# Kernel optimization log

Measured on AMD Instinct MI355X. Metric: run time of the kernel, lower is better.

The kernel has to match this reference:

```python
import jax, jax.numpy as jnp
import numpy as np

NEG_SLOPE = 0.2

def gat_layer(x, W, al, ar, src, dst, n_dst):
    # x: [Ns, Fin]; W: [Fin, H*D]; al/ar: [H, D]; src/dst: [E]
    H, D = al.shape
    h = (x @ W).reshape(-1, H, D)          # [Ns, H, D]
    h_dst = h[:n_dst]                       # dst nodes are prefix of src nodes (DGL block)
    el = (h * al).sum(-1)                   # [Ns, H]
    er = (h_dst * ar).sum(-1)               # [Nd, H]
    e = jax.nn.leaky_relu(el[src] + er[dst], NEG_SLOPE)  # [E, H]
    m = jax.ops.segment_max(e, dst, num_segments=n_dst)  # stable edge-softmax
    a = jnp.exp(e - m[dst])
    s = jax.ops.segment_sum(a, dst, num_segments=n_dst)
    alpha = a / s[dst]                      # [E, H]
    msg = h[src] * alpha[:, :, None]        # [E, H, D]
    out = jax.ops.segment_sum(msg, dst, num_segments=n_dst)  # [Nd, H, D]
    return out.reshape(n_dst, H * D)


def setup_inputs() -> dict:
    key = jax.random.key(0)
    ks = jax.random.split(key, 16)
    N0, N1, N2, N3 = 200000, 100000, 50000, 25000
    E0, E1, E2 = 1000000, 500000, 250000
    Fin, Dh, H, C = 256, 64, 3, 40
    inp = {}
    inp['x'] = jax.random.normal(ks[0], (N0, Fin), jnp.float32)
    inp['src0'] = jax.random.randint(ks[1], (E0,), 0, N0, jnp.int32)
    inp['dst0'] = jnp.sort(jax.random.randint(ks[2], (E0,), 0, N1, jnp.int32))
    inp['src1'] = jax.random.randint(ks[3], (E1,), 0, N1, jnp.int32)
    inp['dst1'] = jnp.sort(jax.random.randint(ks[4], (E1,), 0, N2, jnp.int32))
    inp['src2'] = jax.random.randint(ks[5], (E2,), 0, N2, jnp.int32)
    inp['dst2'] = jnp.sort(jax.random.randint(ks[6], (E2,), 0, N3, jnp.int32))
    sc = lambda f: np.float32(1.0 / np.sqrt(f))
    inp['W0'] = jax.random.normal(ks[7], (Fin, H * Dh), jnp.float32) * sc(Fin)
    inp['al0'] = jax.random.normal(ks[8], (H, Dh), jnp.float32) * sc(Dh)
    inp['ar0'] = jax.random.normal(ks[9], (H, Dh), jnp.float32) * sc(Dh)
    inp['W1'] = jax.random.normal(ks[10], (H * Dh, H * Dh), jnp.float32) * sc(H * Dh)
    inp['al1'] = jax.random.normal(ks[11], (H, Dh), jnp.float32) * sc(Dh)
    inp['ar1'] = jax.random.normal(ks[12], (H, Dh), jnp.float32) * sc(Dh)
    inp['W2'] = jax.random.normal(ks[13], (H * Dh, C), jnp.float32) * sc(H * Dh)
    inp['al2'] = jax.random.normal(ks[14], (1, C), jnp.float32) * sc(C)
    inp['ar2'] = jax.random.normal(ks[15], (1, C), jnp.float32) * sc(C)
    return inp


def reference(x, src0, dst0, src1, dst1, src2, dst2,
              W0, al0, ar0, W1, al1, ar1, W2, al2, ar2):
    N1, N2, N3 = 100000, 50000, 25000
    h = gat_layer(x, W0, al0, ar0, src0, dst0, N1)
    h = jax.nn.relu(h)  # dropout is identity in eval/deterministic mode
    h = gat_layer(h, W1, al1, ar1, src1, dst1, N2)
    h = jax.nn.relu(h)
    out = gat_layer(h, W2, al2, ar2, src2, dst2, N3)  # [N3, n_classes]
    return out
```

## Files before the change

### kernel.cpp

```cpp
#include <hip/hip_runtime.h>
#include <math.h>

#define DEV_INLINE __device__ __forceinline__

typedef __attribute__((ext_vector_type(8))) short short8v;
typedef __attribute__((ext_vector_type(4))) float float4v;

DEV_INLINE unsigned short f2bf_rtn(float f) {
  unsigned u = __float_as_uint(f);
  u += 0x7FFFu + ((u >> 16) & 1u);
  return (unsigned short)(u >> 16);
}
DEV_INLINE float bf2f(unsigned short s) { return __uint_as_float(((unsigned)s) << 16); }

DEV_INLINE int soff(int row, int oct) { return row * 32 + ((oct ^ ((row >> 1) & 3)) << 3); }

__global__ void conv_w_all(const float* __restrict__ W0, const float* __restrict__ W1,
                           const float* __restrict__ W2, short* __restrict__ w0h,
                           short* __restrict__ w0l, short* __restrict__ w1h,
                           short* __restrict__ w1l, short* __restrict__ w2h,
                           short* __restrict__ w2l) {
  const int S0 = 256 * 192, S1 = 192 * 192, S2 = 192 * 40;
  int idx = blockIdx.x * 256 + threadIdx.x;
  const float* W; short *Wh, *Wl; int K;
  if (idx < S0) { W = W0; Wh = w0h; Wl = w0l; K = 256; }
  else if (idx < S0 + S1) { idx -= S0; W = W1; Wh = w1h; Wl = w1l; K = 192; }
  else if (idx < S0 + S1 + S2) { idx -= S0 + S1; W = W2; Wh = w2h; Wl = w2l; K = 192; }
  else return;
  int n = idx / K, k = idx - n * K;
  int N = (W == W0 || W == W1) ? 192 : 40;
  float w = W[(size_t)k * N + n];
  unsigned short h = f2bf_rtn(w);
  Wh[idx] = (short)h;
  Wl[idx] = (short)f2bf_rtn(w - bf2f(h));
}

__global__ void csr_all(const int* __restrict__ d0, const int* __restrict__ d1,
                        const int* __restrict__ d2, int* __restrict__ o0,
                        int* __restrict__ o1, int* __restrict__ o2,
                        int E0, int E1, int E2, int n1, int n2, int n3) {
  int i = blockIdx.x * 256 + threadIdx.x;
  const int* dst; int* off; int E, nd;
  if (i < E0) { dst = d0; off = o0; E = E0; nd = n1; }
  else if (i < E0 + E1) { i -= E0; dst = d1; off = o1; E = E1; nd = n2; }
  else if (i < E0 + E1 + E2) { i -= E0 + E1; dst = d2; off = o2; E = E2; nd = n3; }
  else return;
  int d = dst[i];
  int p = (i == 0) ? -1 : dst[i - 1];
  for (int q = p + 1; q <= d; ++q) off[q] = i;
  if (i == E - 1)
    for (int q = d + 1; q <= nd; ++q) off[q] = E;
}

#define ISSUE_B(k0)                                                           \
  {                                                                           \
    _Pragma("unroll")                                                         \
    for (int q = 0; q < BREP; ++q) {                                          \
      int n = sr + q * 64;                                                    \
      if (n < BN) {                                                           \
        if (n < N) {                                                          \
          pbh[q] = *(const short8v*)(Bth + (size_t)n * K + (k0) + oct * 8);   \
          pbl[q] = *(const short8v*)(Btl + (size_t)n * K + (k0) + oct * 8);   \
        } else {                                                              \
          _Pragma("unroll")                                                   \
          for (int j = 0; j < 8; ++j) { pbh[q][j] = 0; pbl[q][j] = 0; }       \
        }                                                                     \
      }                                                                       \
    }                                                                         \
  }

#define STAGE_B(buf)                                                          \
  {                                                                           \
    _Pragma("unroll")                                                         \
    for (int q = 0; q < BREP; ++q) {                                          \
      int n = sr + q * 64;                                                    \
      if (n < BN) {                                                           \
        *(short8v*)(Bs_h[buf] + soff(n, oct)) = pbh[q];                       \
        *(short8v*)(Bs_l[buf] + soff(n, oct)) = pbl[q];                       \
      }                                                                       \
    }                                                                         \
  }

template <int NT, int H>
__global__ __launch_bounds__(256) void gemm_fused(
    const float* __restrict__ A, const short* __restrict__ Bth,
    const short* __restrict__ Btl, const float* __restrict__ al,
    const float* __restrict__ ar, float* __restrict__ C,
    float* __restrict__ el, float* __restrict__ er,
    int M, int N, int K, int n_dst) {
  constexpr int BN = NT * 16;
  constexpr int BREP = (BN + 63) / 64;
  constexpr int TPH = NT / H;
  __shared__ short Bs_h[2][BN * 32], Bs_l[2][BN * 32];
  const int tid = threadIdx.x;
  const int w = tid >> 6, lane = tid & 63;
  const int quad = lane >> 4, l16 = lane & 15;
  const int m0 = blockIdx.x * 128;

  float4v acc[2][NT];
#pragma unroll
  for (int mt = 0; mt < 2; ++mt)
#pragma unroll
    for (int nt = 0; nt < NT; ++nt)
#pragma unroll
      for (int r = 0; r < 4; ++r) acc[mt][nt][r] = 0.f;

  const int sr = tid >> 2;
  const int oct = tid & 3;

  short8v pbh[BREP], pbl[BREP];

  const int nk = K >> 5;
  ISSUE_B(0);
  STAGE_B(0);
  if (nk > 1) ISSUE_B(32);
  __syncthreads();

  for (int kt = 0; kt < nk; ++kt) {
    const int cur = kt & 1;
    const int k0 = kt << 5;
    float4 fA[2][2];
#pragma unroll
    for (int mt = 0; mt < 2; ++mt) {
      int row = m0 + w * 32 + mt * 16 + l16;
      if (row < M) {
        const float* ap = A + (size_t)row * K + k0 + quad * 8;
        fA[mt][0] = *(const float4*)ap;
        fA[mt][1] = *(const float4*)(ap + 4);
      } else {
        fA[mt][0] = make_float4(0.f, 0.f, 0.f, 0.f);
        fA[mt][1] = fA[mt][0];
      }
    }
    if (kt + 1 < nk) STAGE_B(cur ^ 1);
    if (kt + 2 < nk) ISSUE_B((kt + 2) << 5);
    short8v afh[2], afl[2];
#pragma unroll
    for (int mt = 0; mt < 2; ++mt) {
      float vs[8] = {fA[mt][0].x, fA[mt][0].y, fA[mt][0].z, fA[mt][0].w,
                     fA[mt][1].x, fA[mt][1].y, fA[mt][1].z, fA[mt][1].w};
#pragma unroll
      for (int j = 0; j < 8; ++j) {
        unsigned short hh = f2bf_rtn(vs[j]);
        afh[mt][j] = (short)hh;
        afl[mt][j] = (short)f2bf_rtn(vs[j] - bf2f(hh));
      }
    }
#pragma unroll
    for (int nt = 0; nt < NT; ++nt) {
      int col = nt * 16 + l16;
      short8v bfh = *(const short8v*)(Bs_h[cur] + soff(col, quad));
      short8v bfl = *(const short8v*)(Bs_l[cur] + soff(col, quad));
#pragma unroll
      for (int mt = 0; mt < 2; ++mt) {
        acc[mt][nt] = __builtin_amdgcn_mfma_f32_16x16x32_bf16(afh[mt], bfh, acc[mt][nt], 0, 0, 0);
        acc[mt][nt] = __builtin_amdgcn_mfma_f32_16x16x32_bf16(afh[mt], bfl, acc[mt][nt], 0, 0, 0);
        acc[mt][nt] = __builtin_amdgcn_mfma_f32_16x16x32_bf16(afl[mt], bfh, acc[mt][nt], 0, 0, 0);
      }
    }
    if (kt + 1 < nk) __syncthreads();
  }

  float av[NT], rv[NT];
#pragma unroll
  for (int nt = 0; nt < NT; ++nt) {
    int col = nt * 16 + l16;
    av[nt] = (col < N) ? al[col] : 0.f;
    rv[nt] = (col < N) ? ar[col] : 0.f;
  }
#pragma unroll
  for (int mt = 0; mt < 2; ++mt)
#pragma unroll
    for (int r = 0; r < 4; ++r) {
      int gm = m0 + w * 32 + mt * 16 + quad * 4 + r;
      if (gm >= M) continue;
      float pl[H], pr[H];
#pragma unroll
      for (int h = 0; h < H; ++h) { pl[h] = 0.f; pr[h] = 0.f; }
#pragma unroll
      for (int nt = 0; nt < NT; ++nt) {
        int h = nt / TPH;
        pl[h] = fmaf(acc[mt][nt][r], av[nt], pl[h]);
        pr[h] = fmaf(acc[mt][nt][r], rv[nt], pr[h]);
      }
#pragma unroll
      for (int h = 0; h < H; ++h) {
#pragma unroll
        for (int o = 8; o >= 1; o >>= 1) {
          pl[h] += __shfl_xor(pl[h], o, 16);
          pr[h] += __shfl_xor(pr[h], o, 16);
        }
      }
      if (l16 == 0) {
#pragma unroll
        for (int h = 0; h < H; ++h) {
          el[gm * H + h] = pl[h];
          if (gm < n_dst) er[gm * H + h] = pr[h];
        }
      }
#pragma unroll
      for (int nt = 0; nt < NT; ++nt) {
        int col = nt * 16 + l16;
        if (col < N) C[(size_t)gm * N + col] = acc[mt][nt][r];
      }
    }
}

template <int H, int D, bool RELU>
__global__ __launch_bounds__(256) void agg2_kernel(
    const float* __restrict__ hsrc, const float* __restrict__ el,
    const float* __restrict__ er, const int* __restrict__ src,
    const int* __restrict__ off, float* __restrict__ out, int n_dst) {
  constexpr int F = H * D;
  constexpr int NP = (F + 63) / 64;
  __shared__ float wbuf[16][16][H];
  __shared__ int sbuf[16][16];
  const int g = threadIdx.x >> 4, l = threadIdx.x & 15;
  const int d = blockIdx.x * 16 + g;
  if (d >= n_dst) return;
  const int lo = off[d], hi = off[d + 1];

  if (hi <= lo) {
#pragma unroll
    for (int p = 0; p < NP; ++p) {
      int c4 = (p * 16 + l) * 4;
      if (c4 < F) *(float4*)(out + (size_t)d * F + c4) = make_float4(0.f, 0.f, 0.f, 0.f);
    }
    return;
  }

  float erv[H], s_part[H];
#pragma unroll
  for (int h = 0; h < H; ++h) {
    erv[h] = er[d * H + h];
    s_part[h] = 0.f;
  }
  float4 acc[NP];
#pragma unroll
  for (int p = 0; p < NP; ++p) acc[p] = make_float4(0.f, 0.f, 0.f, 0.f);

  for (int base = lo; base < hi; base += 16) {
    const int i = base + l;
    const bool valid = i < hi;
    const int sid = valid ? src[i] : 0;
#pragma unroll
    for (int h = 0; h < H; ++h) {
      float e = 0.f;
      if (valid) {
        e = el[sid * H + h] + erv[h];
        e = e > 0.f ? e : 0.2f * e;
        e = __expf(e);
      }
      s_part[h] += e;
      wbuf[g][l][h] = e;
    }
    sbuf[g][l] = sid;

    const int cnt = min(16, hi - base);
    int sj = sbuf[g][0];
    float4 hv[NP], hn[NP];
#pragma unroll
    for (int p = 0; p < NP; ++p) {
      int c4 = (p * 16 + l) * 4;
      hv[p] = (c4 < F) ? *(const float4*)(hsrc + (size_t)sj * F + c4)
                       : make_float4(0.f, 0.f, 0.f, 0.f);
    }
    for (int ei = 0; ei < cnt; ++ei) {
      if (ei + 1 < cnt) {
        int sj2 = sbuf[g][ei + 1];
#pragma unroll
        for (int p = 0; p < NP; ++p) {
          int c4 = (p * 16 + l) * 4;
          hn[p] = (c4 < F) ? *(const float4*)(hsrc + (size_t)sj2 * F + c4)
                           : make_float4(0.f, 0.f, 0.f, 0.f);
        }
      }
#pragma unroll
      for (int p = 0; p < NP; ++p) {
        int c4 = (p * 16 + l) * 4;
        float wc = wbuf[g][ei][c4 / D];
        acc[p].x = fmaf(wc, hv[p].x, acc[p].x);
        acc[p].y = fmaf(wc, hv[p].y, acc[p].y);
        acc[p].z = fmaf(wc, hv[p].z, acc[p].z);
        acc[p].w = fmaf(wc, hv[p].w, acc[p].w);
      }
#pragma unroll
      for (int p = 0; p < NP; ++p) hv[p] = hn[p];
    }
  }

#pragma unroll
  for (int h = 0; h < H; ++h)
#pragma unroll
    for (int o = 8; o >= 1; o >>= 1) s_part[h] += __shfl_xor(s_part[h], o, 16);

#pragma unroll
  for (int p = 0; p < NP; ++p) {
    int c4 = (p * 16 + l) * 4;
    if (c4 < F) {
      float inv = 1.f / s_part[c4 / D];
      float4 o;
      o.x = acc[p].x * inv; o.y = acc[p].y * inv;
      o.z = acc[p].z * inv; o.w = acc[p].w * inv;
      if (RELU) {
        o.x = fmaxf(o.x, 0.f); o.y = fmaxf(o.y, 0.f);
        o.z = fmaxf(o.z, 0.f); o.w = fmaxf(o.w, 0.f);
      }
      *(float4*)(out + (size_t)d * F + c4) = o;
    }
  }
}

extern "C" void kernel_launch(void* const* d_in, const int* in_sizes, int n_in,
                              void* d_out, int out_size, void* d_ws, size_t ws_size,
                              hipStream_t stream) {
  const float* x   = (const float*)d_in[0];
  const int* src0  = (const int*)d_in[1];
  const int* dst0  = (const int*)d_in[2];
  const int* src1  = (const int*)d_in[3];
  const int* dst1  = (const int*)d_in[4];
  const int* src2  = (const int*)d_in[5];
  const int* dst2  = (const int*)d_in[6];
  const float* W0  = (const float*)d_in[7];
  const float* al0 = (const float*)d_in[8];
  const float* ar0 = (const float*)d_in[9];
  const float* W1  = (const float*)d_in[10];
  const float* al1 = (const float*)d_in[11];
  const float* ar1 = (const float*)d_in[12];
  const float* W2  = (const float*)d_in[13];
  const float* al2 = (const float*)d_in[14];
  const float* ar2 = (const float*)d_in[15];

  const int N0 = 200000, N1 = 100000, N2 = 50000, N3 = 25000;
  const int E0 = in_sizes[1], E1 = in_sizes[3], E2 = in_sizes[5];
  const int Fin = 256, F = 192, C = 40;

  float* ws     = (float*)d_ws;
  float* h_buf  = ws;
  float* o_buf  = h_buf + (size_t)N0 * F;
  float* el_buf = o_buf + (size_t)N1 * F;
  float* er_buf = el_buf + (size_t)N0 * 3;
  short* w0h    = (short*)(er_buf + (size_t)N1 * 3);
  short* w0l    = w0h + 192 * 256;
  short* w1h    = w0l + 192 * 256;
  short* w1l    = w1h + 192 * 192;
  short* w2h    = w1l + 192 * 192;
  short* w2l    = w2h + 40 * 192;
  int*   off0   = (int*)(w2l + 40 * 192);
  int*   off1   = off0 + (N1 + 1);
  int*   off2   = off1 + (N2 + 1);

  dim3 blk(256);

  const int WTOT = 256 * 192 + 192 * 192 + 192 * 40;
  conv_w_all<<<dim3((WTOT + 255) / 256), blk, 0, stream>>>(W0, W1, W2, w0h, w0l, w1h, w1l, w2h, w2l);
  const int ETOT = E0 + E1 + E2;
  csr_all<<<dim3((ETOT + 255) / 256), blk, 0, stream>>>(dst0, dst1, dst2, off0, off1, off2,
                                                        E0, E1, E2, N1, N2, N3);

  gemm_fused<12, 3><<<dim3((N0 + 127) / 128), blk, 0, stream>>>(
      x, w0h, w0l, al0, ar0, h_buf, el_buf, er_buf, N0, F, Fin, N1);
  agg2_kernel<3, 64, true><<<dim3((N1 + 15) / 16), blk, 0, stream>>>(
      h_buf, el_buf, er_buf, src0, off0, o_buf, N1);

  gemm_fused<12, 3><<<dim3((N1 + 127) / 128), blk, 0, stream>>>(
      o_buf, w1h, w1l, al1, ar1, h_buf, el_buf, er_buf, N1, F, F, N2);
  agg2_kernel<3, 64, true><<<dim3((N2 + 15) / 16), blk, 0, stream>>>(
      h_buf, el_buf, er_buf, src1, off1, o_buf, N2);

  gemm_fused<3, 1><<<dim3((N2 + 127) / 128), blk, 0, stream>>>(
      o_buf, w2h, w2l, al2, ar2, h_buf, el_buf, er_buf, N2, C, F, N3);
  agg2_kernel<1, 40, false><<<dim3((N3 + 15) / 16), blk, 0, stream>>>(
      h_buf, el_buf, er_buf, src2, off2, (float*)d_out, N3);
}
```

Baseline: 662.4 us.

## Load GEMM weight tiles directly into LDS via global_load_lds DMA

Replaces the register-staged B-tile loads (global to registers, then registers to LDS, with two-deep prefetch) with direct global-to-LDS loads using global_load_lds. The swizzle is folded into the per-lane global offset. The last-layer weights are padded to 48 columns so the DMA needs no bounds check. It also adds an occupancy hint of 3 blocks per CU, aiming to cut register pressure and LDS store instructions. The prefetch depth drops to one tile, and correctness depends on the hidden sync and swizzle matching the LDS layout.

```diff
diff --git a/kernel.cpp b/kernel.cpp
--- a/kernel.cpp
+++ b/kernel.cpp
@@ -14,21 +14,29 @@
 DEV_INLINE float bf2f(unsigned short s) { return __uint_as_float(((unsigned)s) << 16); }
 
 DEV_INLINE int soff(int row, int oct) { return row * 32 + ((oct ^ ((row >> 1) & 3)) << 3); }
+
+DEV_INLINE void gload_lds16(const void* g, void* l) {
+  __builtin_amdgcn_global_load_lds(
+      (const __attribute__((address_space(1))) void*)g,
+      (__attribute__((address_space(3))) void*)l, 16, 0, 0);
+}
 
 __global__ void conv_w_all(const float* __restrict__ W0, const float* __restrict__ W1,
                            const float* __restrict__ W2, short* __restrict__ w0h,
                            short* __restrict__ w0l, short* __restrict__ w1h,
                            short* __restrict__ w1l, short* __restrict__ w2h,
                            short* __restrict__ w2l) {
-  const int S0 = 256 * 192, S1 = 192 * 192, S2 = 192 * 40;
+  const int S0 = 256 * 192, S1 = 192 * 192, S2 = 192 * 48;
   int idx = blockIdx.x * 256 + threadIdx.x;
   const float* W; short *Wh, *Wl; int K;
-  if (idx < S0) { W = W0; Wh = w0h; Wl = w0l; K = 256; }
-  else if (idx < S0 + S1) { idx -= S0; W = W1; Wh = w1h; Wl = w1l; K = 192; }
-  else if (idx < S0 + S1 + S2) { idx -= S0 + S1; W = W2; Wh = w2h; Wl = w2l; K = 192; }
+  int which;
+  if (idx < S0) { W = W0; Wh = w0h; Wl = w0l; K = 256; which = 0; }
+  else if (idx < S0 + S1) { idx -= S0; W = W1; Wh = w1h; Wl = w1l; K = 192; which = 1; }
+  else if (idx < S0 + S1 + S2) { idx -= S0 + S1; W = W2; Wh = w2h; Wl = w2l; K = 192; which = 2; }
   else return;
   int n = idx / K, k = idx - n * K;
-  int N = (W == W0 || W == W1) ? 192 : 40;
+  if (which == 2 && n >= 40) { Wh[idx] = 0; Wl[idx] = 0; return; }
+  int N = (which == 2) ? 40 : 192;
   float w = W[(size_t)k * N + n];
   unsigned short h = f2bf_rtn(w);
   Wh[idx] = (short)h;
@@ -52,44 +60,25 @@
     for (int q = d + 1; q <= nd; ++q) off[q] = E;
 }
 
-#define ISSUE_B(k0)                                                           \
+#define DMA_B(ktv, bufv)                                                      \
   {                                                                           \
-    _Pragma("unroll")                                                         \
-    for (int q = 0; q < BREP; ++q) {                                          \
-      int n = sr + q * 64;                                                    \
-      if (n < BN) {                                                           \
-        if (n < N) {                                                          \
-          pbh[q] = *(const short8v*)(Bth + (size_t)n * K + (k0) + oct * 8);   \
-          pbl[q] = *(const short8v*)(Btl + (size_t)n * K + (k0) + oct * 8);   \
-        } else {                                                              \
-          _Pragma("unroll")                                                   \
-          for (int j = 0; j < 8; ++j) { pbh[q][j] = 0; pbl[q][j] = 0; }       \
-        }                                                                     \
-      }                                                                       \
+    const int kb = (ktv) << 6;                                \
+    for (int c = w; c < NT; c += 4) {                                         \
+      gload_lds16((const char*)Bth + (size_t)c * (K * 32) + voff + kb,        \
+                  (short*)Bs_h[bufv] + c * 512);                              \
+      gload_lds16((const char*)Btl + (size_t)c * (K * 32) + voff + kb,        \
+                  (short*)Bs_l[bufv] + c * 512);                              \
     }                                                                         \
   }
 
-#define STAGE_B(buf)                                                          \
-  {                                                                           \
-    _Pragma("unroll")                                                         \
-    for (int q = 0; q < BREP; ++q) {                                          \
-      int n = sr + q * 64;                                                    \
-      if (n < BN) {                                                           \
-        *(short8v*)(Bs_h[buf] + soff(n, oct)) = pbh[q];                       \
-        *(short8v*)(Bs_l[buf] + soff(n, oct)) = pbl[q];                       \
-      }                                                                       \
-    }                                                                         \
-  }
-
 template <int NT, int H>
-__global__ __launch_bounds__(256) void gemm_fused(
+__global__ __launch_bounds__(256, 3) void gemm_fused(
     const float* __restrict__ A, const short* __restrict__ Bth,
     const short* __restrict__ Btl, const float* __restrict__ al,
     const float* __restrict__ ar, float* __restrict__ C,
     float* __restrict__ el, float* __restrict__ er,
     int M, int N, int K, int n_dst) {
   constexpr int BN = NT * 16;
-  constexpr int BREP = (BN + 63) / 64;
   constexpr int TPH = NT / H;
   __shared__ short Bs_h[2][BN * 32], Bs_l[2][BN * 32];
   const int tid = threadIdx.x;
@@ -97,6 +86,8 @@
   const int quad = lane >> 4, l16 = lane & 15;
   const int m0 = blockIdx.x * 128;
 
+  const int voff = (lane >> 2) * (K * 2) + ((((lane & 3) ^ ((lane >> 3) & 3))) << 4);
+
   float4v acc[2][NT];
 #pragma unroll
   for (int mt = 0; mt < 2; ++mt)
@@ -105,40 +96,31 @@
 #pragma unroll
       for (int r = 0; r < 4; ++r) acc[mt][nt][r] = 0.f;
 
-  const int sr = tid >> 2;
-  const int oct = tid & 3;
-
-  short8v pbh[BREP], pbl[BREP];
-
   const int nk = K >> 5;
-  ISSUE_B(0);
-  STAGE_B(0);
-  if (nk > 1) ISSUE_B(32);
+  DMA_B(0, 0);
   __syncthreads();
 
   for (int kt = 0; kt < nk; ++kt) {
     const int cur = kt & 1;
-    const int k0 = kt << 5;
-    float4 fA[2][2];
+    float4 xa[2][2];
 #pragma unroll
     for (int mt = 0; mt < 2; ++mt) {
       int row = m0 + w * 32 + mt * 16 + l16;
       if (row < M) {
-        const float* ap = A + (size_t)row * K + k0 + quad * 8;
-        fA[mt][0] = *(const float4*)ap;
-        fA[mt][1] = *(const float4*)(ap + 4);
+        const float* ap = A + (size_t)row * K + (kt << 5) + quad * 8;
+        xa[mt][0] = *(const float4*)ap;
+        xa[mt][1] = *(const float4*)(ap + 4);
       } else {
-        fA[mt][0] = make_float4(0.f, 0.f, 0.f, 0.f);
-        fA[mt][1] = fA[mt][0];
-      }
-    }
-    if (kt + 1 < nk) STAGE_B(cur ^ 1);
-    if (kt + 2 < nk) ISSUE_B((kt + 2) << 5);
+        xa[mt][0] = make_float4(0.f, 0.f, 0.f, 0.f);
+        xa[mt][1] = xa[mt][0];
+      }
+    }
+    if (kt + 1 < nk) DMA_B(kt + 1, cur ^ 1);
     short8v afh[2], afl[2];
 #pragma unroll
     for (int mt = 0; mt < 2; ++mt) {
-      float vs[8] = {fA[mt][0].x, fA[mt][0].y, fA[mt][0].z, fA[mt][0].w,
-                     fA[mt][1].x, fA[mt][1].y, fA[mt][1].z, fA[mt][1].w};
+      float vs[8] = {xa[mt][0].x, xa[mt][0].y, xa[mt][0].z, xa[mt][0].w,
+                     xa[mt][1].x, xa[mt][1].y, xa[mt][1].z, xa[mt][1].w};
 #pragma unroll
       for (int j = 0; j < 8; ++j) {
         unsigned short hh = f2bf_rtn(vs[j]);
@@ -345,14 +327,14 @@
   short* w1h    = w0l + 192 * 256;
   short* w1l    = w1h + 192 * 192;
   short* w2h    = w1l + 192 * 192;
-  short* w2l    = w2h + 40 * 192;
-  int*   off0   = (int*)(w2l + 40 * 192);
+  short* w2l    = w2h + 48 * 192;
+  int*   off0   = (int*)(w2l + 48 * 192);
   int*   off1   = off0 + (N1 + 1);
   int*   off2   = off1 + (N2 + 1);
 
   dim3 blk(256);
 
-  const int WTOT = 256 * 192 + 192 * 192 + 192 * 40;
+  const int WTOT = 256 * 192 + 192 * 192 + 192 * 48;
   conv_w_all<<<dim3((WTOT + 255) / 256), blk, 0, stream>>>(W0, W1, W2, w0h, w0l, w1h, w1l, w2h, w2l);
   const int ETOT = E0 + E1 + E2;
   csr_all<<<dim3((ETOT + 255) / 256), blk, 0, stream>>>(dst0, dst1, dst2, off0, off1, off2,
```

After: 637.8 us. 3.7% less time.
